# Kernel tuning notes

Hardware: AMD Instinct MI355X
Metric: run time of the kernel (lower is better)

Reference implementation:

```python
import jax, jax.numpy as jnp
import numpy as np

EPS = 1e-5

def conv2d(x, w, stride=1, pad=0, groups=1):
    return jax.lax.conv_general_dilated(
        x, w, (stride, stride), [(pad, pad), (pad, pad)],
        feature_group_count=groups,
        dimension_numbers=('NCHW', 'OIHW', 'NCHW'))

def prelu(x, a):
    return jnp.where(x > 0, x, a[None, :, None, None] * x)

def batchnorm(x, g, b):
    # training-mode BN: batch statistics over N,H,W (biased variance, as torch)
    m = jnp.mean(x, axis=(0, 2, 3), keepdims=True)
    v = jnp.var(x, axis=(0, 2, 3), keepdims=True)
    xhat = (x - m) * jax.lax.rsqrt(v + EPS)
    return xhat * g[None, :, None, None] + b[None, :, None, None]

def setup_inputs() -> dict:
    key = jax.random.key(0)
    ks = jax.random.split(key, 8)
    C_in, C_out, stride = 128, 256, 2
    x = jax.random.normal(ks[0], (32, C_in, 56, 56), dtype=jnp.float32)
    w1 = jax.random.normal(ks[1], (C_out, C_in, 1, 1), dtype=jnp.float32) * 0.05
    w_dw = jax.random.normal(ks[2], (C_out, 1, 3, 3), dtype=jnp.float32) * 0.1
    w3 = jax.random.normal(ks[3], (C_out, C_out, 1, 1), dtype=jnp.float32) * 0.05
    w_adj = jax.random.normal(ks[4], (C_out, C_in, 1, 1), dtype=jnp.float32) * 0.05
    a_init = jnp.full((C_out,), 0.25, dtype=jnp.float32)  # PReLU init
    ones = jnp.ones((C_out,), dtype=jnp.float32)
    zeros = jnp.zeros((C_out,), dtype=jnp.float32)
    return {
        'x': x,
        'w1': w1, 'a1': a_init, 'g1': ones, 'b1': zeros,
        'w_dw': w_dw, 'a2': a_init, 'g2': ones, 'b2': zeros,
        'w3': w3, 'a3': a_init, 'g3': ones, 'b3': zeros,
        'w_adj': w_adj,
    }

def reference(x, w1, a1, g1, b1, w_dw, a2, g2, b2, w3, a3, g3, b3, w_adj):
    stride, C_out = 2, w_dw.shape[0]
    residual = conv2d(x, w_adj, stride=stride)  # full-precision shortcut
    xs = jnp.sign(x)
    # binary 1x1 conv (sign(x) already signed; sign is idempotent)
    out = conv2d(jnp.sign(xs), jnp.sign(w1))
    out = batchnorm(prelu(out, a1), g1, b1)
    # binary depthwise 3x3, stride, pad 1
    out = conv2d(jnp.sign(out), jnp.sign(w_dw), stride=stride, pad=1, groups=C_out)
    out = batchnorm(prelu(out, a2), g2, b2)
    # binary 1x1 conv
    out = conv2d(jnp.sign(out), jnp.sign(w3))
    out = batchnorm(prelu(out, a3), g3, b3)
    return out + residual
```

## Files before the change

kernel.cpp:

```cpp
#include <hip/hip_runtime.h>
#include <stdint.h>

#define NB   32
#define CIN  128
#define COUT 256
#define HH   56
#define WW   56
#define S1   (HH*WW)
#define HO   28
#define WO   28
#define S2   (HO*WO)
#define NS1  (NB*S1)
#define NS2  (NB*S2)
#define TOT2 (NS2*COUT)
#define EPSV 1e-5f

constexpr size_t OFF_XBITS = 0;
constexpr size_t OFF_WB1   = OFF_XBITS + (size_t)NS1*8*4;
constexpr size_t OFF_WB3   = OFF_WB1 + 256*8*4;
constexpr size_t OFF_WDW   = OFF_WB3 + 256*16*4;
constexpr size_t OFF_ACC   = OFF_WDW + 4096;
constexpr size_t OFF_THR   = OFF_ACC + 3*256*4*sizeof(int);
constexpr size_t OFF_WBADJ = OFF_THR + 4*256*sizeof(int);
constexpr size_t OFF_XG    = OFF_WBADJ + (size_t)COUT*CIN*2;
constexpr size_t OFF_OUT1  = OFF_XG + (size_t)NS2*CIN*2;
constexpr size_t OFF_OUT2  = OFF_OUT1 + (size_t)NS1*COUT;
constexpr size_t OFF_XB2   = OFF_OUT2 + (size_t)TOT2;
constexpr size_t OFF_OUT3  = OFF_XB2 + (size_t)NS2*16*4;

typedef __attribute__((ext_vector_type(8))) short bf16x8;
typedef __attribute__((ext_vector_type(4))) float f32x4;

__device__ __forceinline__ uint32_t f2bf(float v) {
  uint32_t u = __float_as_uint(v);
  return (u + 0x7fffu + ((u >> 16) & 1u)) >> 16;
}

__device__ __forceinline__ void bn_finalize(const int* __restrict__ acc4,
                                            float a, float g, float b, float inv_ns,
                                            float& sc, float& sh) {
  float ps = (float)acc4[0];
  float ng = (float)acc4[1];
  float pq = (float)acc4[2];
  float nq = (float)acc4[3];
  float mean = (ps + a*ng) * inv_ns;
  float ex2  = (pq + a*a*nq) * inv_ns;
  float var  = ex2 - mean*mean;
  float rs   = rsqrtf(var + EPSV);
  sc = rs * g;
  sh = b - mean * sc;
}

__global__ __launch_bounds__(256) void packx_kernel(
    const float* __restrict__ x, uint32_t* __restrict__ xbits,
    uint32_t* __restrict__ xg,
    const float* __restrict__ w1, const float* __restrict__ w3,
    const float* __restrict__ wdw, const float* __restrict__ wadj,
    uint32_t* __restrict__ wb1, uint32_t* __restrict__ wb3,
    int8_t* __restrict__ wdws, uint32_t* __restrict__ wbadj,
    int* __restrict__ accbase) {
  int wdx = blockIdx.y;
  if (wdx == 0 && blockIdx.x < 256 && threadIdx.x < 64) {
    int co = blockIdx.x;
    int l  = threadIdx.x;
    if (l < 12) {
      int set = l >> 2, k = l & 3;
      accbase[set*1024 + co*4 + k] = 0;
    }
    for (int h = 0; h < 2; ++h) {
      float v = w1[(size_t)co*CIN + h*64 + l];
      unsigned long long bp = __ballot(v > 0.f);
      unsigned long long bn = __ballot(v < 0.f);
      if (l == 0) {
        wb1[co*8 + 2*h    ] = (uint32_t)bp;
        wb1[co*8 + 2*h + 1] = (uint32_t)(bp >> 32);
        wb1[co*8 + 4 + 2*h    ] = (uint32_t)bn;
        wb1[co*8 + 4 + 2*h + 1] = (uint32_t)(bn >> 32);
      }
    }
    for (int h = 0; h < 4; ++h) {
      float v = w3[(size_t)co*COUT + h*64 + l];
      unsigned long long bp = __ballot(v > 0.f);
      unsigned long long bn = __ballot(v < 0.f);
      if (l == 0) {
        wb3[co*16 + 2*h    ] = (uint32_t)bp;
        wb3[co*16 + 2*h + 1] = (uint32_t)(bp >> 32);
        wb3[co*16 + 8 + 2*h    ] = (uint32_t)bn;
        wb3[co*16 + 8 + 2*h + 1] = (uint32_t)(bn >> 32);
      }
    }
    if (l < 9) {
      float v = wdw[co*9 + l];
      wdws[co*9 + l] = (int8_t)((v > 0.f) - (v < 0.f));
    }
    {
      float v0 = wadj[(size_t)co*CIN + 2*l];
      float v1 = wadj[(size_t)co*CIN + 2*l + 1];
      wbadj[co*64 + l] = f2bf(v0) | (f2bf(v1) << 16);
    }
  }

  int m = blockIdx.x*256 + threadIdx.x;
  int n = m / S1, hw = m % S1;
  size_t base = ((size_t)n*CIN + wdx*32)*S1 + hw;
  uint32_t p = 0, q = 0;
  uint32_t bv[16];
  #pragma unroll
  for (int j = 0; j < 32; ++j) {
    float v = x[base + (size_t)j*S1];
    p |= (uint32_t)(v > 0.f) << j;
    q |= (uint32_t)(v < 0.f) << j;
    uint32_t b = f2bf(v);
    if (j & 1) bv[j >> 1] |= b << 16; else bv[j >> 1] = b;
  }
  xbits[(size_t)m*8 + wdx    ] = p;
  xbits[(size_t)m*8 + 4 + wdx] = q;
  int h = hw / WW, w = hw % WW;
  if (((h | w) & 1) == 0) {
    int m2 = n*S2 + (h >> 1)*WO + (w >> 1);
    uint4* dst = (uint4*)(xg + (size_t)m2*64 + wdx*16);
    dst[0] = make_uint4(bv[0],  bv[1],  bv[2],  bv[3]);
    dst[1] = make_uint4(bv[4],  bv[5],  bv[6],  bv[7]);
    dst[2] = make_uint4(bv[8],  bv[9],  bv[10], bv[11]);
    dst[3] = make_uint4(bv[12], bv[13], bv[14], bv[15]);
  }
}

__global__ __launch_bounds__(256) void conv1_kernel(
    const uint32_t* __restrict__ xb, const uint32_t* __restrict__ wb,
    int8_t* __restrict__ out1) {
  int m = blockIdx.x*256 + threadIdx.x;
  int n = m / S1, hw = m % S1;
  const uint32_t* xw = xb + (size_t)m*8;
  uint32_t p0 = xw[0], p1 = xw[1], p2 = xw[2], p3 = xw[3];
  uint32_t q0 = xw[4], q1 = xw[5], q2 = xw[6], q3 = xw[7];
  int co0 = blockIdx.y * 32;
  size_t obase = ((size_t)n*COUT)*S1 + hw;
  bool nozero = (((p0|q0) & (p1|q1) & (p2|q2) & (p3|q3)) == 0xffffffffu);
  if (nozero) {
    #pragma unroll 4
    for (int co = co0; co < co0 + 32; ++co) {
      const uint32_t* w8 = wb + (size_t)co*8;
      int s = __popc(p0 ^ w8[0]) + __popc(p1 ^ w8[1])
            + __popc(p2 ^ w8[2]) + __popc(p3 ^ w8[3]);
      int acc = 128 - 2*s;
      if (acc > 127) acc = 127;
      out1[obase + (size_t)co*S1] = (int8_t)acc;
    }
  } else {
    #pragma unroll 4
    for (int co = co0; co < co0 + 32; ++co) {
      const uint32_t* w8 = wb + (size_t)co*8;
      uint32_t a0 = w8[0], a1 = w8[1], a2 = w8[2], a3 = w8[3];
      uint32_t b0 = w8[4], b1 = w8[5], b2 = w8[6], b3 = w8[7];
      int acc = __popc(p0&a0) + __popc(p1&a1) + __popc(p2&a2) + __popc(p3&a3)
              + __popc(q0&b0) + __popc(q1&b1) + __popc(q2&b2) + __popc(q3&b3)
              - __popc(p0&b0) - __popc(p1&b1) - __popc(p2&b2) - __popc(p3&b3)
              - __popc(q0&a0) - __popc(q1&a1) - __popc(q2&a2) - __popc(q3&a3);
      if (acc > 127) acc = 127;
      out1[obase + (size_t)co*S1] = (int8_t)acc;
    }
  }
}

__global__ __launch_bounds__(256) void stats_i8_kernel(
    const int8_t* __restrict__ buf, int* __restrict__ accum,
    int s_sp, int quads_per_block) {
  int co = blockIdx.x, slice = blockIdx.y;
  int q0 = slice * quads_per_block;
  int psum = 0, nsum = 0, psq = 0, nsq = 0;
  for (int i = threadIdx.x; i < quads_per_block; i += 256) {
    int flat = (q0 + i) * 4;
    int n = flat / s_sp, hw = flat % s_sp;
    char4 v = *reinterpret_cast<const char4*>(buf + (size_t)(n*COUT + co)*s_sp + hw);
    int vs[4] = {v.x, v.y, v.z, v.w};
    #pragma unroll
    for (int k = 0; k < 4; ++k) {
      int f = vs[k];
      if (f > 0) { psum += f; psq += f*f; } else { nsum += f; nsq += f*f; }
    }
  }
  __shared__ int r0[256], r1[256], r2[256], r3[256];
  int t = threadIdx.x;
  r0[t] = psum; r1[t] = nsum; r2[t] = psq; r3[t] = nsq;
  __syncthreads();
  for (int s = 128; s > 0; s >>= 1) {
    if (t < s) { r0[t]+=r0[t+s]; r1[t]+=r1[t+s]; r2[t]+=r2[t+s]; r3[t]+=r3[t+s]; }
    __syncthreads();
  }
  if (t == 0) {
    atomicAdd(&accum[co*4+0], r0[0]);
    atomicAdd(&accum[co*4+1], r1[0]);
    atomicAdd(&accum[co*4+2], r2[0]);
    atomicAdd(&accum[co*4+3], r3[0]);
  }
}

__global__ __launch_bounds__(256) void stats_i16_kernel(
    const int16_t* __restrict__ buf, int* __restrict__ accum,
    int s_sp, int pairs_per_block) {
  int co = blockIdx.x, slice = blockIdx.y;
  int p0i = slice * pairs_per_block;
  int psum = 0, nsum = 0, psq = 0, nsq = 0;
  for (int i = threadIdx.x; i < pairs_per_block; i += 256) {
    int flat = (p0i + i) * 2;
    int n = flat / s_sp, hw = flat % s_sp;
    short2 v = *reinterpret_cast<const short2*>(buf + (size_t)(n*COUT + co)*s_sp + hw);
    int vs[2] = {v.x, v.y};
    #pragma unroll
    for (int k = 0; k < 2; ++k) {
      int f = vs[k];
      if (f > 0) { psum += f; psq += f*f; } else { nsum += f; nsq += f*f; }
    }
  }
  __shared__ int r0[256], r1[256], r2[256], r3[256];
  int t = threadIdx.x;
  r0[t] = psum; r1[t] = nsum; r2[t] = psq; r3[t] = nsq;
  __syncthreads();
  for (int s = 128; s > 0; s >>= 1) {
    if (t < s) { r0[t]+=r0[t+s]; r1[t]+=r1[t+s]; r2[t]+=r2[t+s]; r3[t]+=r3[t+s]; }
    __syncthreads();
  }
  if (t == 0) {
    atomicAdd(&accum[co*4+0], r0[0]);
    atomicAdd(&accum[co*4+1], r1[0]);
    atomicAdd(&accum[co*4+2], r2[0]);
    atomicAdd(&accum[co*4+3], r3[0]);
  }
}

__global__ __launch_bounds__(256) void thr_kernel(
    const int* __restrict__ accum, const float* __restrict__ a,
    const float* __restrict__ g, const float* __restrict__ b,
    float inv_ns, int vlo, int vhi,
    int* __restrict__ Tpos, int* __restrict__ Tneg) {
  int co = threadIdx.x;
  float av = a[co], sc, sh;
  bn_finalize(accum + co*4, av, g[co], b[co], inv_ns, sc, sh);
  int tp = vhi + 1, tn = vlo - 1;
  for (int v = vlo; v <= vhi; ++v) {
    float f = (float)v;
    float p = f > 0.f ? f : av*f;
    float tv = p*sc + sh;
    if (tv > 0.f && v < tp) tp = v;
    if (tv < 0.f && v > tn) tn = v;
  }
  Tpos[co] = tp;
  Tneg[co] = tn;
}

#define DW_SLABS 8
#define DW_RB    68
__global__ __launch_bounds__(256) void dw_kernel(
    const int8_t* __restrict__ out1, const int8_t* __restrict__ wdws,
    const int* __restrict__ Tp1, const int* __restrict__ Tn1,
    int8_t* __restrict__ out2) {
  __shared__ int8_t sl[DW_SLABS][57][DW_RB];
  int tid = threadIdx.x;
  int nc0 = blockIdx.x * DW_SLABS;

  int* slw = (int*)&sl[0][0][0];
  #pragma unroll
  for (int i = tid; i < DW_SLABS*57*DW_RB/4; i += 256) slw[i] = 0;
  __syncthreads();

  for (int i = tid; i < DW_SLABS*784; i += 256) {
    int slab = i / 784;
    int d    = i - slab*784;
    int ih   = d / 14;
    int iwd  = d - ih*14;
    int co   = (nc0 + slab) & (COUT-1);
    int Tp = Tp1[co], Tn = Tn1[co];
    uint32_t v4 = ((const uint32_t*)(out1 + (size_t)(nc0 + slab)*S1))[d];
    uint32_t s4 = 0;
    #pragma unroll
    for (int k = 0; k < 4; ++k) {
      int v = (int)(int8_t)(v4 >> (8*k));
      int s = (v >= Tp) - (v <= Tn);
      s4 |= (uint32_t)(s & 0xff) << (8*k);
    }
    *(uint32_t*)&sl[slab][ih + 1][4 + 4*iwd] = s4;
  }
  __syncthreads();

  if (tid < DW_SLABS*HO) {
    int slab = tid / HO;
    int ho   = tid - slab*HO;
    int nc = nc0 + slab;
    int co = nc & (COUT-1);
    int wv[9];
    #pragma unroll
    for (int k = 0; k < 9; ++k) wv[k] = wdws[co*9 + k];
    const uint32_t* r0 = (const uint32_t*)&sl[slab][2*ho    ][4];
    const uint32_t* r1 = (const uint32_t*)&sl[slab][2*ho + 1][4];
    const uint32_t* r2 = (const uint32_t*)&sl[slab][2*ho + 2][4];
    uint32_t* o32 = (uint32_t*)(out2 + (size_t)nc*S2 + ho*WO);
    int c0 = 0, c1 = 0, c2 = 0;
    uint32_t obuf = 0;
    #pragma unroll
    for (int q = 0; q < 14; ++q) {
      uint32_t d0 = r0[q], d1 = r1[q], d2 = r2[q];
      int s00=(int)(int8_t)d0, s01=(int)(int8_t)(d0>>8), s02=(int)(int8_t)(d0>>16), s03=(int)(int8_t)(d0>>24);
      int s10=(int)(int8_t)d1, s11=(int)(int8_t)(d1>>8), s12=(int)(int8_t)(d1>>16), s13=(int)(int8_t)(d1>>24);
      int s20=(int)(int8_t)d2, s21=(int)(int8_t)(d2>>8), s22=(int)(int8_t)(d2>>16), s23=(int)(int8_t)(d2>>24);
      int a0 = c0*wv[0] + s00*wv[1] + s01*wv[2]
             + c1*wv[3] + s10*wv[4] + s11*wv[5]
             + c2*wv[6] + s20*wv[7] + s21*wv[8];
      int a1 = s01*wv[0] + s02*wv[1] + s03*wv[2]
             + s11*wv[3] + s12*wv[4] + s13*wv[5]
             + s21*wv[6] + s22*wv[7] + s23*wv[8];
      c0 = s03; c1 = s13; c2 = s23;
      if ((q & 1) == 0) {
        obuf = (uint32_t)(a0 & 0xff) | ((uint32_t)(a1 & 0xff) << 8);
      } else {
        obuf |= ((uint32_t)(a0 & 0xff) << 16) | ((uint32_t)(a1 & 0xff) << 24);
        o32[q >> 1] = obuf;
      }
    }
  }
}

__global__ __launch_bounds__(256) void pack2_kernel(
    const int8_t* __restrict__ out2,
    const int* __restrict__ Tp2, const int* __restrict__ Tn2,
    uint32_t* __restrict__ xb2) {
  int m = blockIdx.x*256 + threadIdx.x;
  int wdx = blockIdx.y;
  int n = m / S2, hw = m % S2;
  uint32_t p = 0, q = 0;
  #pragma unroll
  for (int j = 0; j < 32; ++j) {
    int c = wdx*32 + j;
    int v = out2[(size_t)(n*COUT + c)*S2 + hw];
    p |= (uint32_t)(v >= Tp2[c]) << j;
    q |= (uint32_t)(v <= Tn2[c]) << j;
  }
  xb2[(size_t)m*16 + wdx    ] = p;
  xb2[(size_t)m*16 + 8 + wdx] = q;
}

__global__ __launch_bounds__(256) void conv3_kernel(
    const uint32_t* __restrict__ xb2, const uint32_t* __restrict__ wb3,
    int16_t* __restrict__ out3) {
  int m = blockIdx.x*256 + threadIdx.x;
  int n = m / S2, hw = m % S2;
  const uint32_t* xw = xb2 + (size_t)m*16;
  uint32_t P[8], Q[8];
  #pragma unroll
  for (int i = 0; i < 8; ++i) { P[i] = xw[i]; Q[i] = xw[8+i]; }
  int co0 = blockIdx.y * 32;
  size_t obase = ((size_t)n*COUT)*S2 + hw;
  uint32_t allm = 0xffffffffu;
  #pragma unroll
  for (int i = 0; i < 8; ++i) allm &= (P[i] | Q[i]);
  if (allm == 0xffffffffu) {
    #pragma unroll 2
    for (int co = co0; co < co0 + 32; ++co) {
      const uint32_t* w = wb3 + (size_t)co*16;
      int s = 0;
      #pragma unroll
      for (int i = 0; i < 8; ++i) s += __popc(P[i] ^ w[i]);
      out3[obase + (size_t)co*S2] = (int16_t)(256 - 2*s);
    }
  } else {
    #pragma unroll 2
    for (int co = co0; co < co0 + 32; ++co) {
      const uint32_t* w = wb3 + (size_t)co*16;
      int acc = 0;
      #pragma unroll
      for (int i = 0; i < 8; ++i) {
        uint32_t wp = w[i], wn = w[8+i];
        acc += __popc(P[i]&wp) + __popc(Q[i]&wn) - __popc(P[i]&wn) - __popc(Q[i]&wp);
      }
      out3[obase + (size_t)co*S2] = (int16_t)acc;
    }
  }
}

__global__ __launch_bounds__(256) void resfinal_kernel(
    const uint16_t* __restrict__ xg, const uint16_t* __restrict__ wb,
    const int16_t* __restrict__ out3,
    const float* __restrict__ a3, const float* __restrict__ g3,
    const float* __restrict__ b3, const int* __restrict__ acc3,
    float* __restrict__ out) {
  int lane = threadIdx.x & 63;
  int wid  = threadIdx.x >> 6;
  int m0  = blockIdx.x*64 + wid*16;
  int co0 = blockIdx.y*64;
  int r16 = lane & 15, hi = lane >> 4;
  int koff = hi * 8;

  const bf16x8* arow = (const bf16x8*)(xg + (size_t)(m0 + r16)*CIN + koff);
  bf16x8 af0 = arow[0], af1 = arow[4], af2 = arow[8], af3 = arow[12];

  f32x4 d0, d1, d2, d3;
  {
    const bf16x8* brow = (const bf16x8*)(wb + (size_t)(co0 + r16)*CIN + koff);
    f32x4 a = {0.f,0.f,0.f,0.f};
    a = __builtin_amdgcn_mfma_f32_16x16x32_bf16(af0, brow[0],  a, 0,0,0);
    a = __builtin_amdgcn_mfma_f32_16x16x32_bf16(af1, brow[4],  a, 0,0,0);
    a = __builtin_amdgcn_mfma_f32_16x16x32_bf16(af2, brow[8],  a, 0,0,0);
    a = __builtin_amdgcn_mfma_f32_16x16x32_bf16(af3, brow[12], a, 0,0,0);
    d0 = a;
  }
  {
    const bf16x8* brow = (const bf16x8*)(wb + (size_t)(co0 + 16 + r16)*CIN + koff);
    f32x4 a = {0.f,0.f,0.f,0.f};
    a = __builtin_amdgcn_mfma_f32_16x16x32_bf16(af0, brow[0],  a, 0,0,0);
    a = __builtin_amdgcn_mfma_f32_16x16x32_bf16(af1, brow[4],  a, 0,0,0);
    a = __builtin_amdgcn_mfma_f32_16x16x32_bf16(af2, brow[8],  a, 0,0,0);
    a = __builtin_amdgcn_mfma_f32_16x16x32_bf16(af3, brow[12], a, 0,0,0);
    d1 = a;
  }
  {
    const bf16x8* brow = (const bf16x8*)(wb + (size_t)(co0 + 32 + r16)*CIN + koff);
    f32x4 a = {0.f,0.f,0.f,0.f};
    a = __builtin_amdgcn_mfma_f32_16x16x32_bf16(af0, brow[0],  a, 0,0,0);
    a = __builtin_amdgcn_mfma_f32_16x16x32_bf16(af1, brow[4],  a, 0,0,0);
    a = __builtin_amdgcn_mfma_f32_16x16x32_bf16(af2, brow[8],  a, 0,0,0);
    a = __builtin_amdgcn_mfma_f32_16x16x32_bf16(af3, brow[12], a, 0,0,0);
    d2 = a;
  }
  {
    const bf16x8* brow = (const bf16x8*)(wb + (size_t)(co0 + 48 + r16)*CIN + koff);
    f32x4 a = {0.f,0.f,0.f,0.f};
    a = __builtin_amdgcn_mfma_f32_16x16x32_bf16(af0, brow[0],  a, 0,0,0);
    a = __builtin_amdgcn_mfma_f32_16x16x32_bf16(af1, brow[4],  a, 0,0,0);
    a = __builtin_amdgcn_mfma_f32_16x16x32_bf16(af2, brow[8],  a, 0,0,0);
    a = __builtin_amdgcn_mfma_f32_16x16x32_bf16(af3, brow[12], a, 0,0,0);
    d3 = a;
  }

  int mrow = m0 + hi*4;
  int n  = mrow / S2;
  int hw = mrow - n*S2;
  f32x4 dd[4] = {d0, d1, d2, d3};
  #pragma unroll
  for (int t = 0; t < 4; ++t) {
    int co = co0 + t*16 + r16;
    float av = a3[co], sc, sh;
    bn_finalize(acc3 + co*4, av, g3[co], b3[co], 1.f/NS2, sc, sh);
    size_t o = ((size_t)n*COUT + co)*S2 + hw;
    #pragma unroll
    for (int r = 0; r < 4; ++r) {
      float f = (float)out3[o + r];
      float pp = f > 0.f ? f : av*f;
      out[o + r] = pp*sc + sh + dd[t][r];
    }
  }
}

extern "C" void kernel_launch(void* const* d_in, const int* in_sizes, int n_in,
                              void* d_out, int out_size, void* d_ws, size_t ws_size,
                              hipStream_t stream) {
  (void)in_sizes; (void)n_in; (void)out_size; (void)ws_size;
  const float* x    = (const float*)d_in[0];
  const float* w1   = (const float*)d_in[1];
  const float* a1   = (const float*)d_in[2];
  const float* g1   = (const float*)d_in[3];
  const float* b1   = (const float*)d_in[4];
  const float* wdw  = (const float*)d_in[5];
  const float* a2   = (const float*)d_in[6];
  const float* g2   = (const float*)d_in[7];
  const float* b2   = (const float*)d_in[8];
  const float* w3   = (const float*)d_in[9];
  const float* a3   = (const float*)d_in[10];
  const float* g3   = (const float*)d_in[11];
  const float* b3   = (const float*)d_in[12];
  const float* wadj = (const float*)d_in[13];
  float* out = (float*)d_out;

  char* ws = (char*)d_ws;
  uint32_t* xbits = (uint32_t*)(ws + OFF_XBITS);
  uint32_t* wb1   = (uint32_t*)(ws + OFF_WB1);
  uint32_t* wb3   = (uint32_t*)(ws + OFF_WB3);
  int8_t*   wdws  = (int8_t*)  (ws + OFF_WDW);
  int*      acc1  = (int*)     (ws + OFF_ACC);
  int*      acc2  = acc1 + 256*4;
  int*      acc3  = acc2 + 256*4;
  int*      thr   = (int*)     (ws + OFF_THR);
  int*      Tp1 = thr, *Tn1 = thr + 256, *Tp2 = thr + 512, *Tn2 = thr + 768;
  uint32_t* wbadj = (uint32_t*)(ws + OFF_WBADJ);
  uint32_t* xg    = (uint32_t*)(ws + OFF_XG);
  int8_t*   out1  = (int8_t*)  (ws + OFF_OUT1);
  int8_t*   out2  = (int8_t*)  (ws + OFF_OUT2);
  uint32_t* xb2   = (uint32_t*)(ws + OFF_XB2);
  int16_t*  out3  = (int16_t*) (ws + OFF_OUT3);

  packx_kernel<<<dim3(NS1/256, 4), 256, 0, stream>>>(
      x, xbits, xg, w1, w3, wdw, wadj, wb1, wb3, wdws, wbadj, acc1);
  conv1_kernel<<<dim3(NS1/256, 8), 256, 0, stream>>>(xbits, wb1, out1);
  stats_i8_kernel<<<dim3(256, 8), 256, 0, stream>>>(out1, acc1, S1, 3136);
  thr_kernel<<<1, 256, 0, stream>>>(acc1, a1, g1, b1, 1.f/NS1, -128, 127, Tp1, Tn1);
  dw_kernel<<<NB*COUT/DW_SLABS, 256, 0, stream>>>(out1, wdws, Tp1, Tn1, out2);
  stats_i8_kernel<<<dim3(256, 4), 256, 0, stream>>>(out2, acc2, S2, 1568);
  thr_kernel<<<1, 256, 0, stream>>>(acc2, a2, g2, b2, 1.f/NS2, -9, 9, Tp2, Tn2);
  pack2_kernel<<<dim3(NS2/256, 8), 256, 0, stream>>>(out2, Tp2, Tn2, xb2);
  conv3_kernel<<<dim3(NS2/256, 8), 256, 0, stream>>>(xb2, wb3, out3);
  stats_i16_kernel<<<dim3(256, 4), 256, 0, stream>>>(out3, acc3, S2, 3136);
  resfinal_kernel<<<dim3(NS2/64, COUT/64), 256, 0, stream>>>(
      (const uint16_t*)xg, (const uint16_t*)wbadj, out3, a3, g3, b3, acc3, out);
}
```

Before: 133.2 us.

## Fuse BN threshold and stage-2 stats into dw/pack2; widen stats loads

Removes both thr_kernel launches by having dw_kernel and pack2_kernel compute BN thresholds per block from the accumulated statistics. The separate stats pass over out2 is dropped because dw_kernel now accumulates the sums in shared memory and adds them to the global accumulator with atomics. The stats kernels switch from 4-byte to 16-byte vector loads with fewer blocks. This cuts launches and a full reread of out2, at the cost of computing thresholds redundantly in every block and adding extra atomic traffic.

```diff
diff --git a/kernel.cpp b/kernel.cpp
--- a/kernel.cpp
+++ b/kernel.cpp
@@ -20,8 +20,7 @@
 constexpr size_t OFF_WB3   = OFF_WB1 + 256*8*4;
 constexpr size_t OFF_WDW   = OFF_WB3 + 256*16*4;
 constexpr size_t OFF_ACC   = OFF_WDW + 4096;
-constexpr size_t OFF_THR   = OFF_ACC + 3*256*4*sizeof(int);
-constexpr size_t OFF_WBADJ = OFF_THR + 4*256*sizeof(int);
+constexpr size_t OFF_WBADJ = OFF_ACC + 3*256*4*sizeof(int);
 constexpr size_t OFF_XG    = OFF_WBADJ + (size_t)COUT*CIN*2;
 constexpr size_t OFF_OUT1  = OFF_XG + (size_t)NS2*CIN*2;
 constexpr size_t OFF_OUT2  = OFF_OUT1 + (size_t)NS1*COUT;
@@ -165,19 +164,22 @@
 
 __global__ __launch_bounds__(256) void stats_i8_kernel(
     const int8_t* __restrict__ buf, int* __restrict__ accum,
-    int s_sp, int quads_per_block) {
+    int s_sp, int v16_per_block) {
   int co = blockIdx.x, slice = blockIdx.y;
-  int q0 = slice * quads_per_block;
+  int base16 = slice * v16_per_block;
   int psum = 0, nsum = 0, psq = 0, nsq = 0;
-  for (int i = threadIdx.x; i < quads_per_block; i += 256) {
-    int flat = (q0 + i) * 4;
+  for (int i = threadIdx.x; i < v16_per_block; i += 256) {
+    int flat = (base16 + i) * 16;
     int n = flat / s_sp, hw = flat % s_sp;
-    char4 v = *reinterpret_cast<const char4*>(buf + (size_t)(n*COUT + co)*s_sp + hw);
-    int vs[4] = {v.x, v.y, v.z, v.w};
-    #pragma unroll
-    for (int k = 0; k < 4; ++k) {
-      int f = vs[k];
-      if (f > 0) { psum += f; psq += f*f; } else { nsum += f; nsq += f*f; }
+    int4 v = *reinterpret_cast<const int4*>(buf + (size_t)(n*COUT + co)*s_sp + hw);
+    int ws[4] = {v.x, v.y, v.z, v.w};
+    #pragma unroll
+    for (int d = 0; d < 4; ++d) {
+      #pragma unroll
+      for (int k = 0; k < 4; ++k) {
+        int f = (int)(int8_t)(ws[d] >> (8*k));
+        if (f > 0) { psum += f; psq += f*f; } else { nsum += f; nsq += f*f; }
+      }
     }
   }
   __shared__ int r0[256], r1[256], r2[256], r3[256];
@@ -198,19 +200,21 @@
 
 __global__ __launch_bounds__(256) void stats_i16_kernel(
     const int16_t* __restrict__ buf, int* __restrict__ accum,
-    int s_sp, int pairs_per_block) {
+    int s_sp, int v8_per_block) {
   int co = blockIdx.x, slice = blockIdx.y;
-  int p0i = slice * pairs_per_block;
+  int base8 = slice * v8_per_block;
   int psum = 0, nsum = 0, psq = 0, nsq = 0;
-  for (int i = threadIdx.x; i < pairs_per_block; i += 256) {
-    int flat = (p0i + i) * 2;
+  for (int i = threadIdx.x; i < v8_per_block; i += 256) {
+    int flat = (base8 + i) * 8;
     int n = flat / s_sp, hw = flat % s_sp;
-    short2 v = *reinterpret_cast<const short2*>(buf + (size_t)(n*COUT + co)*s_sp + hw);
-    int vs[2] = {v.x, v.y};
-    #pragma unroll
-    for (int k = 0; k < 2; ++k) {
-      int f = vs[k];
-      if (f > 0) { psum += f; psq += f*f; } else { nsum += f; nsq += f*f; }
+    int4 v = *reinterpret_cast<const int4*>(buf + (size_t)(n*COUT + co)*s_sp + hw);
+    int ws[4] = {v.x, v.y, v.z, v.w};
+    #pragma unroll
+    for (int d = 0; d < 4; ++d) {
+      int lo = (int)(short)(ws[d] & 0xffff);
+      int hi = (int)(short)(ws[d] >> 16);
+      if (lo > 0) { psum += lo; psq += lo*lo; } else { nsum += lo; nsq += lo*lo; }
+      if (hi > 0) { psum += hi; psq += hi*hi; } else { nsum += hi; nsq += hi*hi; }
     }
   }
   __shared__ int r0[256], r1[256], r2[256], r3[256];
@@ -229,39 +233,45 @@
   }
 }
 
-__global__ __launch_bounds__(256) void thr_kernel(
-    const int* __restrict__ accum, const float* __restrict__ a,
-    const float* __restrict__ g, const float* __restrict__ b,
-    float inv_ns, int vlo, int vhi,
-    int* __restrict__ Tpos, int* __restrict__ Tneg) {
-  int co = threadIdx.x;
-  float av = a[co], sc, sh;
-  bn_finalize(accum + co*4, av, g[co], b[co], inv_ns, sc, sh);
-  int tp = vhi + 1, tn = vlo - 1;
-  for (int v = vlo; v <= vhi; ++v) {
-    float f = (float)v;
-    float p = f > 0.f ? f : av*f;
-    float tv = p*sc + sh;
-    if (tv > 0.f && v < tp) tp = v;
-    if (tv < 0.f && v > tn) tn = v;
-  }
-  Tpos[co] = tp;
-  Tneg[co] = tn;
-}
-
 #define DW_SLABS 8
 #define DW_RB    68
 __global__ __launch_bounds__(256) void dw_kernel(
     const int8_t* __restrict__ out1, const int8_t* __restrict__ wdws,
-    const int* __restrict__ Tp1, const int* __restrict__ Tn1,
-    int8_t* __restrict__ out2) {
+    const int* __restrict__ acc1, const float* __restrict__ a1,
+    const float* __restrict__ g1, const float* __restrict__ b1,
+    int8_t* __restrict__ out2, int* __restrict__ accum2) {
   __shared__ int8_t sl[DW_SLABS][57][DW_RB];
+  __shared__ int sTp[DW_SLABS], sTn[DW_SLABS], sAcc[DW_SLABS][4];
   int tid = threadIdx.x;
   int nc0 = blockIdx.x * DW_SLABS;
+  int co0 = nc0 & (COUT-1);
 
   int* slw = (int*)&sl[0][0][0];
   #pragma unroll
   for (int i = tid; i < DW_SLABS*57*DW_RB/4; i += 256) slw[i] = 0;
+  if (tid < DW_SLABS) { sTp[tid] = 128; sTn[tid] = -129; }
+  if (tid < DW_SLABS*4) sAcc[tid >> 2][tid & 3] = 0;
+  __syncthreads();
+
+  {
+    int slab = tid >> 5;
+    int co = co0 + slab;
+    float av = a1[co], sc, sh;
+    bn_finalize(acc1 + co*4, av, g1[co], b1[co], 1.f/NS1, sc, sh);
+    int tp = 128, tn = -129;
+    int v0 = -128 + (tid & 31)*8;
+    #pragma unroll
+    for (int k = 0; k < 8; ++k) {
+      int v = v0 + k;
+      float f = (float)v;
+      float pr = f > 0.f ? f : av*f;
+      float tv = pr*sc + sh;
+      if (tv > 0.f && v < tp) tp = v;
+      if (tv < 0.f && v > tn) tn = v;
+    }
+    atomicMin(&sTp[slab], tp);
+    atomicMax(&sTn[slab], tn);
+  }
   __syncthreads();
 
   for (int i = tid; i < DW_SLABS*784; i += 256) {
@@ -269,8 +279,7 @@
     int d    = i - slab*784;
     int ih   = d / 14;
     int iwd  = d - ih*14;
-    int co   = (nc0 + slab) & (COUT-1);
-    int Tp = Tp1[co], Tn = Tn1[co];
+    int Tp = sTp[slab], Tn = sTn[slab];
     uint32_t v4 = ((const uint32_t*)(out1 + (size_t)(nc0 + slab)*S1))[d];
     uint32_t s4 = 0;
     #pragma unroll
@@ -283,17 +292,18 @@
   }
   __syncthreads();
 
+  int psum = 0, nsum = 0, psq = 0, nsq = 0;
+  int slabD = tid / HO;
   if (tid < DW_SLABS*HO) {
-    int slab = tid / HO;
-    int ho   = tid - slab*HO;
-    int nc = nc0 + slab;
-    int co = nc & (COUT-1);
+    int ho   = tid - slabD*HO;
+    int nc = nc0 + slabD;
+    int co = co0 + slabD;
     int wv[9];
     #pragma unroll
     for (int k = 0; k < 9; ++k) wv[k] = wdws[co*9 + k];
-    const uint32_t* r0 = (const uint32_t*)&sl[slab][2*ho    ][4];
-    const uint32_t* r1 = (const uint32_t*)&sl[slab][2*ho + 1][4];
-    const uint32_t* r2 = (const uint32_t*)&sl[slab][2*ho + 2][4];
+    const uint32_t* r0 = (const uint32_t*)&sl[slabD][2*ho    ][4];
+    const uint32_t* r1 = (const uint32_t*)&sl[slabD][2*ho + 1][4];
+    const uint32_t* r2 = (const uint32_t*)&sl[slabD][2*ho + 2][4];
     uint32_t* o32 = (uint32_t*)(out2 + (size_t)nc*S2 + ho*WO);
     int c0 = 0, c1 = 0, c2 = 0;
     uint32_t obuf = 0;
@@ -306,34 +316,62 @@
       int a0 = c0*wv[0] + s00*wv[1] + s01*wv[2]
              + c1*wv[3] + s10*wv[4] + s11*wv[5]
              + c2*wv[6] + s20*wv[7] + s21*wv[8];
-      int a1 = s01*wv[0] + s02*wv[1] + s03*wv[2]
-             + s11*wv[3] + s12*wv[4] + s13*wv[5]
-             + s21*wv[6] + s22*wv[7] + s23*wv[8];
+      int a1v = s01*wv[0] + s02*wv[1] + s03*wv[2]
+              + s11*wv[3] + s12*wv[4] + s13*wv[5]
+              + s21*wv[6] + s22*wv[7] + s23*wv[8];
       c0 = s03; c1 = s13; c2 = s23;
+      if (a0 > 0) { psum += a0; psq += a0*a0; } else { nsum += a0; nsq += a0*a0; }
+      if (a1v > 0) { psum += a1v; psq += a1v*a1v; } else { nsum += a1v; nsq += a1v*a1v; }
       if ((q & 1) == 0) {
-        obuf = (uint32_t)(a0 & 0xff) | ((uint32_t)(a1 & 0xff) << 8);
+        obuf = (uint32_t)(a0 & 0xff) | ((uint32_t)(a1v & 0xff) << 8);
       } else {
-        obuf |= ((uint32_t)(a0 & 0xff) << 16) | ((uint32_t)(a1 & 0xff) << 24);
+        obuf |= ((uint32_t)(a0 & 0xff) << 16) | ((uint32_t)(a1v & 0xff) << 24);
         o32[q >> 1] = obuf;
       }
     }
+    atomicAdd(&sAcc[slabD][0], psum);
+    atomicAdd(&sAcc[slabD][1], nsum);
+    atomicAdd(&sAcc[slabD][2], psq);
+    atomicAdd(&sAcc[slabD][3], nsq);
+  }
+  __syncthreads();
+
+  if (tid < DW_SLABS*4) {
+    int slab = tid >> 2, k = tid & 3;
+    atomicAdd(&accum2[(co0 + slab)*4 + k], sAcc[slab][k]);
   }
 }
 
 __global__ __launch_bounds__(256) void pack2_kernel(
-    const int8_t* __restrict__ out2,
-    const int* __restrict__ Tp2, const int* __restrict__ Tn2,
-    uint32_t* __restrict__ xb2) {
+    const int8_t* __restrict__ out2, const int* __restrict__ acc2,
+    const float* __restrict__ a2, const float* __restrict__ g2,
+    const float* __restrict__ b2, uint32_t* __restrict__ xb2) {
+  __shared__ int sTp[32], sTn[32];
+  int wdx = blockIdx.y;
+  if (threadIdx.x < 32) {
+    int c = wdx*32 + threadIdx.x;
+    float av = a2[c], sc, sh;
+    bn_finalize(acc2 + c*4, av, g2[c], b2[c], 1.f/NS2, sc, sh);
+    int tp = 10, tn = -10;
+    for (int v = -9; v <= 9; ++v) {
+      float f = (float)v;
+      float pr = f > 0.f ? f : av*f;
+      float tv = pr*sc + sh;
+      if (tv > 0.f && v < tp) tp = v;
+      if (tv < 0.f && v > tn) tn = v;
+    }
+    sTp[threadIdx.x] = tp; sTn[threadIdx.x] = tn;
+  }
+  __syncthreads();
   int m = blockIdx.x*256 + threadIdx.x;
-  int wdx = blockIdx.y;
   int n = m / S2, hw = m % S2;
   uint32_t p = 0, q = 0;
   #pragma unroll
   for (int j = 0; j < 32; ++j) {
     int c = wdx*32 + j;
     int v = out2[(size_t)(n*COUT + c)*S2 + hw];
-    p |= (uint32_t)(v >= Tp2[c]) << j;
-    q |= (uint32_t)(v <= Tn2[c]) << j;
+    p |= (uint32_t)(v >= sTp[j]) << j;
+    q |= (uint32_t)(v <= sTn[j]) << j;
   }
   xb2[(size_t)m*16 + wdx    ] = p;
   xb2[(size_t)m*16 + 8 + wdx] = q;
@@ -478,8 +516,6 @@
   int*      acc1  = (int*)     (ws + OFF_ACC);
   int*      acc2  = acc1 + 256*4;
   int*      acc3  = acc2 + 256*4;
-  int*      thr   = (int*)     (ws + OFF_THR);
-  int*      Tp1 = thr, *Tn1 = thr + 256, *Tp2 = thr + 512, *Tn2 = thr + 768;
   uint32_t* wbadj = (uint32_t*)(ws + OFF_WBADJ);
   uint32_t* xg    = (uint32_t*)(ws + OFF_XG);
   int8_t*   out1  = (int8_t*)  (ws + OFF_OUT1);
@@ -490,14 +526,11 @@
   packx_kernel<<<dim3(NS1/256, 4), 256, 0, stream>>>(
       x, xbits, xg, w1, w3, wdw, wadj, wb1, wb3, wdws, wbadj, acc1);
   conv1_kernel<<<dim3(NS1/256, 8), 256, 0, stream>>>(xbits, wb1, out1);
-  stats_i8_kernel<<<dim3(256, 8), 256, 0, stream>>>(out1, acc1, S1, 3136);
-  thr_kernel<<<1, 256, 0, stream>>>(acc1, a1, g1, b1, 1.f/NS1, -128, 127, Tp1, Tn1);
-  dw_kernel<<<NB*COUT/DW_SLABS, 256, 0, stream>>>(out1, wdws, Tp1, Tn1, out2);
-  stats_i8_kernel<<<dim3(256, 4), 256, 0, stream>>>(out2, acc2, S2, 1568);
-  thr_kernel<<<1, 256, 0, stream>>>(acc2, a2, g2, b2, 1.f/NS2, -9, 9, Tp2, Tn2);
-  pack2_kernel<<<dim3(NS2/256, 8), 256, 0, stream>>>(out2, Tp2, Tn2, xb2);
+  stats_i8_kernel<<<dim3(256, 4), 256, 0, stream>>>(out1, acc1, S1, 1568);
+  dw_kernel<<<NB*COUT/DW_SLABS, 256, 0, stream>>>(out1, wdws, acc1, a1, g1, b1, out2, acc2);
+  pack2_kernel<<<dim3(NS2/256, 8), 256, 0, stream>>>(out2, acc2, a2, g2, b2, xb2);
   conv3_kernel<<<dim3(NS2/256, 8), 256, 0, stream>>>(xb2, wb3, out3);
-  stats_i16_kernel<<<dim3(256, 4), 256, 0, stream>>>(out3, acc3, S2, 3136);
+  stats_i16_kernel<<<dim3(256, 4), 256, 0, stream>>>(out3, acc3, S2, 784);
   resfinal_kernel<<<dim3(NS2/64, COUT/64), 256, 0, stream>>>(
       (const uint16_t*)xg, (const uint16_t*)wbadj, out3, a3, g3, b3, acc3, out);
 }
```

Result: faster. 110.0 us (-17.5%).
